# Performance work log

Hardware: AMD Instinct MI355X
Metric: run time of the kernel (lower is better)

The kernel has to match this reference:

```python
import jax, jax.numpy as jnp
import numpy as np

GAMMA = 0.96875


def setup_inputs() -> dict:
    key = jax.random.key(0)
    kx, kq, kk, kv = jax.random.split(key, 4)
    B, T, D = 4, 2048, 1024
    x = jax.random.normal(kx, (B, T, D), dtype=jnp.float32)
    Wq = jax.random.normal(kq, (D, D), dtype=jnp.float32) * (1.0 / np.sqrt(D))
    Wk = jax.random.normal(kk, (D, D), dtype=jnp.float32) * (1.0 / np.sqrt(D))
    Wv = jax.random.normal(kv, (D, D), dtype=jnp.float32) * (1.0 / np.sqrt(D))
    return {"x": x, "Wq": Wq, "Wk": Wk, "Wv": Wv}


def reference(x, Wq, Wk, Wv):
    # x: [B, T, D_in]; projections are bias-free Dense layers
    B, T, _ = x.shape
    D = Wq.shape[1]
    Q = jnp.einsum("bti,id->btd", x, Wq)  # [B,T,D]
    K = jnp.einsum("bti,id->btd", x, Wk)
    V = jnp.einsum("bti,id->btd", x, Wv)

    gamma = jnp.asarray(GAMMA, x.dtype)

    # Original: s[t] = gamma*s[t-1] + K[:,t,:]^T @ V[:,t,:]   (a [D,D] state,
    # batch is CONTRACTED by the matmul), then only reduce_sum over the last
    # state axis is used. The recurrence is linear, so it collapses exactly to
    # a [D]-vector recurrence with m_t[d] = sum_b K[b,t,d] * (sum_e V[b,t,e]).
    m = jnp.einsum("btd,bt->td", K, V.sum(axis=-1))  # [T,D]

    def step(s, mt):
        s_new = gamma * s + mt
        return s_new, s_new

    # loop runs t = 1..T-1 starting from s = 0; afterwards s[0] = s[1]
    _, states = jax.lax.scan(step, jnp.zeros((D,), x.dtype), m[1:])  # [T-1,D]
    S = jnp.concatenate([states[:1], states], axis=0)  # [T,D]

    # tf.reshape([T,D] -> [-1, T]) is a row-major element scramble, then transpose
    S = S.reshape(-1, T).T  # [T,D] (scrambled, faithful to the original)

    return S[None, :, :] * Q  # broadcast over batch -> [B,T,D]
```

## Files before the change

kernel.cpp:

```cpp
#include <hip/hip_runtime.h>
#include <hip/hip_bf16.h>
#include <cstddef>

#define T_DIM 2048
#define D_DIM 1024
#define GAMMA_F 0.96875f

typedef __attribute__((ext_vector_type(8))) short bf16x8;
typedef __attribute__((ext_vector_type(8))) ushort ushortx8;
typedef __attribute__((ext_vector_type(4))) float f32x4;

#define AS1 __attribute__((address_space(1)))
#define AS3 __attribute__((address_space(3)))

static __device__ inline ushort f2bs(float f) {
    __hip_bfloat16 h = __float2bfloat16(f);
    return *reinterpret_cast<ushort*>(&h);
}

template <int N>
static __device__ __forceinline__ void vm_wait() {
    if constexpr (N == 0)      asm volatile("s_waitcnt vmcnt(0)" ::: "memory");
    else if constexpr (N == 2) asm volatile("s_waitcnt vmcnt(2)" ::: "memory");
    else if constexpr (N == 3) asm volatile("s_waitcnt vmcnt(3)" ::: "memory");
    else if constexpr (N == 4) asm volatile("s_waitcnt vmcnt(4)" ::: "memory");
    else if constexpr (N == 6) asm volatile("s_waitcnt vmcnt(6)" ::: "memory");
    else if constexpr (N == 8) asm volatile("s_waitcnt vmcnt(8)" ::: "memory");
    else static_assert(N <= 8, "vmcnt");
}
static __device__ __forceinline__ void raw_barrier() {
    asm volatile("s_barrier" ::: "memory");
}

__global__ __launch_bounds__(256) void k_prep(const float* __restrict__ Wk,
                                              const float* __restrict__ Wq,
                                              const float* __restrict__ Wv,
                                              ushort* __restrict__ WTk,
                                              ushort* __restrict__ WTq,
                                              float* __restrict__ wv_sum) {
    const int tid = threadIdx.x;
    if (blockIdx.z == 2) {
        __shared__ float red[4];
        const int i = blockIdx.y * 32 + blockIdx.x;
        const float* row = Wv + (size_t)i * D_DIM;
        float p = 0.f;
        for (int c = tid; c < D_DIM; c += 256) p += row[c];
        for (int o = 32; o; o >>= 1) p += __shfl_down(p, o);
        if ((tid & 63) == 0) red[tid >> 6] = p;
        __syncthreads();
        if (tid == 0) wv_sum[i] = red[0] + red[1] + red[2] + red[3];
        return;
    }
    const float* W = (blockIdx.z == 0) ? Wk : Wq;
    ushort* WT     = (blockIdx.z == 0) ? WTk : WTq;
    __shared__ float tile[32][33];
    const int tx = tid & 31, ty = tid >> 5;
    const int kb = blockIdx.x * 32, nb = blockIdx.y * 32;
    #pragma unroll
    for (int r = 0; r < 4; ++r)
        tile[ty + 8 * r][tx] = W[(size_t)(kb + ty + 8 * r) * 1024 + nb + tx];
    __syncthreads();
    #pragma unroll
    for (int r = 0; r < 4; ++r)
        WT[(size_t)(nb + ty + 8 * r) * 1024 + kb + tx] =
            f2bs(tile[tx][ty + 8 * r]);
}

__global__ __launch_bounds__(256) void k_vsum_y(const float* __restrict__ x,
                                                const float* __restrict__ wv_sum,
                                                ushort* __restrict__ yb,
                                                ushort* __restrict__ xb) {
    __shared__ float xs[4][D_DIM];
    __shared__ float red[4][4];
    const int t = blockIdx.x;
    const int tid = threadIdx.x;
    const int lane = tid & 63, wv = tid >> 6;

    #pragma unroll
    for (int b = 0; b < 4; ++b) {
        const float4* xr = (const float4*)(x + ((size_t)b * T_DIM + t) * D_DIM);
        *(float4*)&xs[b][tid * 4] = xr[tid];
    }
    __syncthreads();

    #pragma unroll
    for (int b = 0; b < 4; ++b) {
        float p = 0.f;
        for (int c = tid; c < D_DIM; c += 256) p += xs[b][c] * wv_sum[c];
        for (int o = 32; o; o >>= 1) p += __shfl_down(p, o);
        if (lane == 0) red[wv][b] = p;
    }
    __syncthreads();

    float vs[4];
    #pragma unroll
    for (int b = 0; b < 4; ++b)
        vs[b] = red[0][b] + red[1][b] + red[2][b] + red[3][b];

    if (tid < 128) {
        const int i0 = tid * 8;
        ushortx8 yv;
        #pragma unroll
        for (int j = 0; j < 8; ++j) {
            float a = 0.f;
            #pragma unroll
            for (int b = 0; b < 4; ++b) a += xs[b][i0 + j] * vs[b];
            yv[j] = f2bs(a);
        }
        *(ushortx8*)(yb + (size_t)t * D_DIM + i0) = yv;
    }
    for (int g = tid; g < 512; g += 256) {
        const int b = g >> 7, i0 = (g & 127) * 8;
        ushortx8 xv;
        #pragma unroll
        for (int j = 0; j < 8; ++j) xv[j] = f2bs(xs[b][i0 + j]);
        *(ushortx8*)(xb + ((size_t)b * T_DIM + t) * D_DIM + i0) = xv;
    }
}

template <int MF, int NF, int EPI>
__global__ __launch_bounds__(512, 4) void k_gemm(const ushort* __restrict__ A,
                                                 const ushort* __restrict__ BT,
                                                 float* __restrict__ C,
                                                 const float* __restrict__ S2) {
    constexpr int BM = 4 * MF * 16;
    constexpr int BN = 2 * NF * 16;
    constexpr int LOADS = BM / 64 + BN / 64;
    __shared__ ushort As[2][BM][64];
    __shared__ ushort Bs[2][BN][64];
    const int tid = threadIdx.x;
    const int lane = tid & 63, wid = tid >> 6;
    const int wr = wid >> 1, wc = wid & 1;
    const int rowBase = blockIdx.x * BM;
    const int colBase = blockIdx.y * BN;

    f32x4 acc[MF][NF];
    #pragma unroll
    for (int i = 0; i < MF; ++i)
        #pragma unroll
        for (int j = 0; j < NF; ++j) acc[i][j] = f32x4{0.f, 0.f, 0.f, 0.f};

    auto stage = [&](int buf, int kb) {
        #pragma unroll
        for (int q = 0; q < BM / 64; ++q) {
            const int s = q * 8192 + tid * 16;
            const int r = s >> 7, grp = (s >> 4) & 7;
            const int gcol = kb + (((grp ^ (r & 7)) & 7) << 3);
            __builtin_amdgcn_global_load_lds(
                (const AS1 void*)(A + (size_t)(rowBase + r) * 1024 + gcol),
                (AS3 void*)((AS3 char*)&As[buf][0][0] + s), 16, 0, 0);
        }
        #pragma unroll
        for (int q = 0; q < BN / 64; ++q) {
            const int s = q * 8192 + tid * 16;
            const int r = s >> 7, grp = (s >> 4) & 7;
            const int gcol = kb + (((grp ^ (r & 7)) & 7) << 3);
            __builtin_amdgcn_global_load_lds(
                (const AS1 void*)(BT + (size_t)(colBase + r) * 1024 + gcol),
                (AS3 void*)((AS3 char*)&Bs[buf][0][0] + s), 16, 0, 0);
        }
    };

    stage(0, 0);

    #pragma unroll 2
    for (int kt = 0; kt < 16; ++kt) {
        const int cur = kt & 1;
        if (kt < 15) {
            stage(cur ^ 1, (kt + 1) * 64);
            vm_wait<LOADS>();
        } else {
            vm_wait<0>();
        }
        raw_barrier();

        bf16x8 af[2][MF], bfv[2][NF];
        #pragma unroll
        for (int ks = 0; ks < 2; ++ks) {
            const int kg = ks * 4 + (lane >> 4);
            #pragma unroll
            for (int mi = 0; mi < MF; ++mi) {
                const int r = wr * (MF * 16) + mi * 16 + (lane & 15);
                af[ks][mi] = *(const bf16x8*)((const char*)&As[cur][0][0] +
                                              r * 128 + (((kg ^ (r & 7)) & 7) << 4));
            }
            #pragma unroll
            for (int ni = 0; ni < NF; ++ni) {
                const int r = wc * (NF * 16) + ni * 16 + (lane & 15);
                bfv[ks][ni] = *(const bf16x8*)((const char*)&Bs[cur][0][0] +
                                               r * 128 + (((kg ^ (r & 7)) & 7) << 4));
            }
        }
        #pragma unroll
        for (int ks = 0; ks < 2; ++ks)
            #pragma unroll
            for (int mi = 0; mi < MF; ++mi)
                #pragma unroll
                for (int ni = 0; ni < NF; ++ni)
                    acc[mi][ni] = __builtin_amdgcn_mfma_f32_16x16x32_bf16(
                        af[ks][mi], bfv[ks][ni], acc[mi][ni], 0, 0, 0);

        asm volatile("s_waitcnt lgkmcnt(0)" ::: "memory");
        raw_barrier();
    }

    #pragma unroll
    for (int mi = 0; mi < MF; ++mi) {
        #pragma unroll
        for (int ni = 0; ni < NF; ++ni) {
            const int col = colBase + wc * (NF * 16) + ni * 16 + (lane & 15);
            #pragma unroll
            for (int q = 0; q < 4; ++q) {
                const int row = rowBase + wr * (MF * 16) + mi * 16 + (lane >> 4) * 4 + q;
                float v = acc[mi][ni][q];
                if (EPI)
                    v *= S2[(size_t)(row & (T_DIM - 1)) * D_DIM + col];
                C[(size_t)row * D_DIM + col] = v;
            }
        }
    }
}

#define SC_L 32
#define SC_NC 64

__global__ __launch_bounds__(256) void k_scan1(const float* __restrict__ m,
                                               float* __restrict__ tot) {
    const int col = blockIdx.x * 64 + (threadIdx.x & 63);
    const int ch  = blockIdx.y * 4 + (threadIdx.x >> 6);
    const int t0 = ch * SC_L;
    float r = 0.f;
    #pragma unroll 4
    for (int k = 0; k < SC_L; ++k) {
        const int t = t0 + k;
        const float a = (t == 0) ? 0.f : m[(size_t)t * D_DIM + col];
        r = GAMMA_F * r + a;
    }
    tot[(size_t)ch * D_DIM + col] = r;
}

__global__ __launch_bounds__(256) void k_scan2(const float* __restrict__ m,
                                               const float* __restrict__ tot,
                                               float* __restrict__ S2) {
    __shared__ float ls[128][65];
    const int tid = threadIdx.x;
    const int cl = tid & 63;
    const int ch = tid >> 6;
    const int col = blockIdx.x * 64 + cl;
    const int chg = blockIdx.y * 4 + ch;
    const int t0 = chg * SC_L;

    float gL = 1.f;
    #pragma unroll
    for (int i = 0; i < SC_L; ++i) gL *= GAMMA_F;

    float carry = 0.f, f = 1.f;
    for (int j = chg - 1; j >= 0; --j) {
        carry += f * tot[(size_t)j * D_DIM + col];
        f *= gL;
    }

    float r = carry, s1 = 0.f;
    #pragma unroll 4
    for (int k = 0; k < SC_L; ++k) {
        const int t = t0 + k;
        const float a = (t == 0) ? 0.f : m[(size_t)t * D_DIM + col];
        r = GAMMA_F * r + a;
        ls[ch * SC_L + k][cl] = r;
        if (t == 1) s1 = r;
    }
    if (blockIdx.y == 0 && ch == 0) ls[0][cl] = s1;
    __syncthreads();

    const int c0 = blockIdx.x * 64;
    const int tB = blockIdx.y * 128;
    for (int e = tid; e < 128 * 64; e += 256) {
        const int rr = e >> 6;
        const int j  = e & 63;
        const int hi = rr >> 6, cl2 = rr & 63;
        S2[(size_t)((hi << 10) + c0 + cl2) * D_DIM + (tB >> 1) + j] =
            ls[2 * j + hi][cl2];
    }
}

extern "C" void kernel_launch(void* const* d_in, const int* in_sizes, int n_in,
                              void* d_out, int out_size, void* d_ws, size_t ws_size,
                              hipStream_t stream) {
    const float* x  = (const float*)d_in[0];
    const float* Wq = (const float*)d_in[1];
    const float* Wk = (const float*)d_in[2];
    const float* Wv = (const float*)d_in[3];
    float* out = (float*)d_out;
    char* ws = (char*)d_ws;

    ushort* xb  = (ushort*)(ws);
    float*  m   = (float*)(ws + (16u << 20));
    ushort* yb  = (ushort*)(ws + (24u << 20));
    ushort* WTk = (ushort*)(ws + (28u << 20));
    ushort* WTq = (ushort*)(ws + (30u << 20));
    float*  S2  = (float*)(ws + (32u << 20));
    float*  wv_sum = m;
    float*  tot = (float*)yb;

    dim3 gP(32, 32, 3);
    k_prep<<<gP, 256, 0, stream>>>(Wk, Wq, Wv, WTk, WTq, wv_sum);

    k_vsum_y<<<T_DIM, 256, 0, stream>>>(x, wv_sum, (ushort*)yb, (ushort*)xb);

    dim3 gm(T_DIM / 128, D_DIM / 64);
    k_gemm<2, 2, 0><<<gm, 512, 0, stream>>>(yb, WTk, m, nullptr);

    dim3 gs(D_DIM / 64, SC_NC / 4);
    k_scan1<<<gs, 256, 0, stream>>>(m, tot);
    k_scan2<<<gs, 256, 0, stream>>>(m, tot, S2);

    dim3 gq((4 * T_DIM) / 128, D_DIM / 128);
    k_gemm<2, 4, 1><<<gq, 512, 0, stream>>>(xb, WTq, out, S2);
}
```

Measured before the change: 80.32 us.

## Add triple-buffered 256x128 GEMM kernel with interleaved loads for Q projection

Replaces the Q-projection GEMM with a new kernel that uses 256x128 output tiles, a three-stage LDS ring buffer filled by direct global-to-LDS loads, and phased MFMA blocks that interleave LDS reads, the next-stage prefetch and s_setprio raises. The aim is more data reuse per tile and better overlap of memory traffic with matrix math in the dominant GEMM. In exchange the larger LDS footprint and register use limit occupancy to two blocks per CU, and the grid is halved along rows. The original GEMM template loses its epilogue parameter and is kept only for the K projection.

```diff
diff --git a/kernel.cpp b/kernel.cpp
--- a/kernel.cpp
+++ b/kernel.cpp
@@ -20,16 +20,20 @@
 
 template <int N>
 static __device__ __forceinline__ void vm_wait() {
+    static_assert(N == 0 || N == 2 || N == 3 || N == 4 || N == 6 || N == 8,
+                  "vm_wait<N>: N not in emitted set");
     if constexpr (N == 0)      asm volatile("s_waitcnt vmcnt(0)" ::: "memory");
     else if constexpr (N == 2) asm volatile("s_waitcnt vmcnt(2)" ::: "memory");
     else if constexpr (N == 3) asm volatile("s_waitcnt vmcnt(3)" ::: "memory");
     else if constexpr (N == 4) asm volatile("s_waitcnt vmcnt(4)" ::: "memory");
     else if constexpr (N == 6) asm volatile("s_waitcnt vmcnt(6)" ::: "memory");
     else if constexpr (N == 8) asm volatile("s_waitcnt vmcnt(8)" ::: "memory");
-    else static_assert(N <= 8, "vmcnt");
 }
 static __device__ __forceinline__ void raw_barrier() {
     asm volatile("s_barrier" ::: "memory");
+}
+static __device__ __forceinline__ void lgkm0() {
+    asm volatile("s_waitcnt lgkmcnt(0)" ::: "memory");
 }
 
 __global__ __launch_bounds__(256) void k_prep(const float* __restrict__ Wk,
@@ -118,11 +122,10 @@
     }
 }
 
-template <int MF, int NF, int EPI>
+template <int MF, int NF>
 __global__ __launch_bounds__(512, 4) void k_gemm(const ushort* __restrict__ A,
                                                  const ushort* __restrict__ BT,
-                                                 float* __restrict__ C,
-                                                 const float* __restrict__ S2) {
+                                                 float* __restrict__ C) {
     constexpr int BM = 4 * MF * 16;
     constexpr int BN = 2 * NF * 16;
     constexpr int LOADS = BM / 64 + BN / 64;
@@ -200,7 +203,7 @@
                     acc[mi][ni] = __builtin_amdgcn_mfma_f32_16x16x32_bf16(
                         af[ks][mi], bfv[ks][ni], acc[mi][ni], 0, 0, 0);
 
-        asm volatile("s_waitcnt lgkmcnt(0)" ::: "memory");
+        lgkm0();
         raw_barrier();
     }
 
@@ -212,6 +215,145 @@
             #pragma unroll
             for (int q = 0; q < 4; ++q) {
                 const int row = rowBase + wr * (MF * 16) + mi * 16 + (lane >> 4) * 4 + q;
+                C[(size_t)row * D_DIM + col] = acc[mi][ni][q];
+            }
+        }
+    }
+}
+
+template <int EPI>
+__global__ __launch_bounds__(512, 2) void k_gemm8(const ushort* __restrict__ A,
+                                                  const ushort* __restrict__ BT,
+                                                  float* __restrict__ C,
+                                                  const float* __restrict__ S2) {
+    constexpr int ABYTES = 256 * 64 * 2;
+    constexpr int BBYTES = 128 * 64 * 2;
+    constexpr int TBYTES = ABYTES + BBYTES;
+    __shared__ char lds[3 * TBYTES];
+    const int tid = threadIdx.x;
+    const int lane = tid & 63, wid = tid >> 6;
+    const int wr = wid >> 1, wc = wid & 1;
+    const int rowBase = blockIdx.x * 256;
+    const int colBase = blockIdx.y * 128;
+
+    f32x4 acc[4][4];
+    #pragma unroll
+    for (int i = 0; i < 4; ++i)
+        #pragma unroll
+        for (int j = 0; j < 4; ++j) acc[i][j] = f32x4{0.f, 0.f, 0.f, 0.f};
+
+    auto stage_part = [&](int buf, int kb, int p) {
+        #pragma unroll
+        for (int qq = 0; qq < 2; ++qq) {
+            const int s = (p * 2 + qq) * 8192 + tid * 16;
+            const int r = s >> 7, grp = (s >> 4) & 7;
+            const int gcol = kb + (((grp ^ (r & 7)) & 7) << 3);
+            __builtin_amdgcn_global_load_lds(
+                (const AS1 void*)(A + (size_t)(rowBase + r) * 1024 + gcol),
+                (AS3 void*)((AS3 char*)lds + buf * TBYTES + s), 16, 0, 0);
+        }
+        {
+            const int s = p * 8192 + tid * 16;
+            const int r = s >> 7, grp = (s >> 4) & 7;
+            const int gcol = kb + (((grp ^ (r & 7)) & 7) << 3);
+            __builtin_amdgcn_global_load_lds(
+                (const AS1 void*)(BT + (size_t)(colBase + r) * 1024 + gcol),
+                (AS3 void*)((AS3 char*)lds + buf * TBYTES + ABYTES + s), 16, 0, 0);
+        }
+    };
+
+    auto rdA = [&](int buf, int mi, int kg) -> bf16x8 {
+        const int r = wr * 64 + mi * 16 + (lane & 15);
+        return *(const bf16x8*)((const char*)lds + buf * TBYTES +
+                                r * 128 + (((kg ^ (r & 7)) & 7) << 4));
+    };
+    auto rdB = [&](int buf, int ni, int kg) -> bf16x8 {
+        const int r = wc * 64 + ni * 16 + (lane & 15);
+        return *(const bf16x8*)((const char*)lds + buf * TBYTES + ABYTES +
+                                r * 128 + (((kg ^ (r & 7)) & 7) << 4));
+    };
+
+    stage_part(0, 0, 0);  stage_part(0, 0, 1);
+    stage_part(1, 64, 0); stage_part(1, 64, 1);
+    vm_wait<6>();
+    raw_barrier();
+
+    const int kg0 = (lane >> 4);
+    const int kg1 = 4 + (lane >> 4);
+    int cur = 0;
+
+    #pragma unroll 1
+    for (int kt = 0; kt < 16; ++kt) {
+        int b2 = cur + 2; if (b2 >= 3) b2 -= 3;
+        const int kb2 = (kt + 2) * 64;
+
+        bf16x8 af[2][4], bfv[2][4];
+
+        af[0][0] = rdA(cur, 0, kg0); af[0][1] = rdA(cur, 1, kg0);
+        af[1][0] = rdA(cur, 0, kg1); af[1][1] = rdA(cur, 1, kg1);
+        bfv[0][0] = rdB(cur, 0, kg0); bfv[0][1] = rdB(cur, 1, kg0);
+        bfv[1][0] = rdB(cur, 0, kg1); bfv[1][1] = rdB(cur, 1, kg1);
+        if (kt < 14) stage_part(b2, kb2, 0);
+        raw_barrier();
+        lgkm0();
+        __builtin_amdgcn_s_setprio(1);
+        #pragma unroll
+        for (int ks = 0; ks < 2; ++ks)
+            #pragma unroll
+            for (int mi = 0; mi < 2; ++mi)
+                #pragma unroll
+                for (int ni = 0; ni < 2; ++ni)
+                    acc[mi][ni] = __builtin_amdgcn_mfma_f32_16x16x32_bf16(
+                        af[ks][mi], bfv[ks][ni], acc[mi][ni], 0, 0, 0);
+        __builtin_amdgcn_s_setprio(0);
+        raw_barrier();
+
+        bfv[0][2] = rdB(cur, 2, kg0); bfv[0][3] = rdB(cur, 3, kg0);
+        bfv[1][2] = rdB(cur, 2, kg1); bfv[1][3] = rdB(cur, 3, kg1);
+        if (kt < 14) stage_part(b2, kb2, 1);
+        raw_barrier();
+        lgkm0();
+        __builtin_amdgcn_s_setprio(1);
+        #pragma unroll
+        for (int ks = 0; ks < 2; ++ks)
+            #pragma unroll
+            for (int mi = 0; mi < 2; ++mi)
+                #pragma unroll
+                for (int ni = 2; ni < 4; ++ni)
+                    acc[mi][ni] = __builtin_amdgcn_mfma_f32_16x16x32_bf16(
+                        af[ks][mi], bfv[ks][ni], acc[mi][ni], 0, 0, 0);
+        __builtin_amdgcn_s_setprio(0);
+        raw_barrier();
+
+        af[0][2] = rdA(cur, 2, kg0); af[0][3] = rdA(cur, 3, kg0);
+        af[1][2] = rdA(cur, 2, kg1); af[1][3] = rdA(cur, 3, kg1);
+        raw_barrier();
+        lgkm0();
+        __builtin_amdgcn_s_setprio(1);
+        #pragma unroll
+        for (int ks = 0; ks < 2; ++ks)
+            #pragma unroll
+            for (int mi = 2; mi < 4; ++mi)
+                #pragma unroll
+                for (int ni = 0; ni < 4; ++ni)
+                    acc[mi][ni] = __builtin_amdgcn_mfma_f32_16x16x32_bf16(
+                        af[ks][mi], bfv[ks][ni], acc[mi][ni], 0, 0, 0);
+        __builtin_amdgcn_s_setprio(0);
+        if (kt < 14)       vm_wait<6>();
+        else if (kt == 14) vm_wait<0>();
+        raw_barrier();
+
+        cur += 1; if (cur == 3) cur = 0;
+    }
+
+    #pragma unroll
+    for (int mi = 0; mi < 4; ++mi) {
+        #pragma unroll
+        for (int ni = 0; ni < 4; ++ni) {
+            const int col = colBase + wc * 64 + ni * 16 + (lane & 15);
+            #pragma unroll
+            for (int q = 0; q < 4; ++q) {
+                const int row = rowBase + wr * 64 + mi * 16 + (lane >> 4) * 4 + q;
                 float v = acc[mi][ni][q];
                 if (EPI)
                     v *= S2[(size_t)(row & (T_DIM - 1)) * D_DIM + col];
@@ -308,12 +450,12 @@
     k_vsum_y<<<T_DIM, 256, 0, stream>>>(x, wv_sum, (ushort*)yb, (ushort*)xb);
 
     dim3 gm(T_DIM / 128, D_DIM / 64);
-    k_gemm<2, 2, 0><<<gm, 512, 0, stream>>>(yb, WTk, m, nullptr);
+    k_gemm<2, 2><<<gm, 512, 0, stream>>>(yb, WTk, m);
 
     dim3 gs(D_DIM / 64, SC_NC / 4);
     k_scan1<<<gs, 256, 0, stream>>>(m, tot);
     k_scan2<<<gs, 256, 0, stream>>>(m, tot, S2);
 
-    dim3 gq((4 * T_DIM) / 128, D_DIM / 128);
-    k_gemm<2, 4, 1><<<gq, 512, 0, stream>>>(xb, WTq, out, S2);
-}
+    dim3 gq((4 * T_DIM) / 256, D_DIM / 128);
+    k_gemm8<1><<<gq, 512, 0, stream>>>(xb, WTq, out, S2);
+}
```

New measurement: 81.61 us. No clear change (+1.6%).

## Merge two-pass chunked scan into one kernel with redundant prefix recompute

Applied to the files above, without the earlier changes.

Replaces the two-kernel chunked scan (per-chunk totals, then carry propagation) with a single kernel where each thread recomputes its carry by scanning m serially from t=1 up to its chunk start. This removes one kernel launch and the intermediate totals buffer. In exchange, work grows quadratically with chunk index: late chunks serially read up to about 2048 rows per column, which lengthens the critical path, and the redundant reads go through cache.

```diff
diff --git a/kernel.cpp b/kernel.cpp
--- a/kernel.cpp
+++ b/kernel.cpp
@@ -20,16 +20,20 @@
 
 template <int N>
 static __device__ __forceinline__ void vm_wait() {
+    static_assert(N == 0 || N == 2 || N == 3 || N == 4 || N == 6 || N == 8,
+                  "vm_wait<N>: N not in emitted set");
     if constexpr (N == 0)      asm volatile("s_waitcnt vmcnt(0)" ::: "memory");
     else if constexpr (N == 2) asm volatile("s_waitcnt vmcnt(2)" ::: "memory");
     else if constexpr (N == 3) asm volatile("s_waitcnt vmcnt(3)" ::: "memory");
     else if constexpr (N == 4) asm volatile("s_waitcnt vmcnt(4)" ::: "memory");
     else if constexpr (N == 6) asm volatile("s_waitcnt vmcnt(6)" ::: "memory");
     else if constexpr (N == 8) asm volatile("s_waitcnt vmcnt(8)" ::: "memory");
-    else static_assert(N <= 8, "vmcnt");
 }
 static __device__ __forceinline__ void raw_barrier() {
     asm volatile("s_barrier" ::: "memory");
+}
+static __device__ __forceinline__ void lgkm0() {
+    asm volatile("s_waitcnt lgkmcnt(0)" ::: "memory");
 }
 
 __global__ __launch_bounds__(256) void k_prep(const float* __restrict__ Wk,
@@ -200,7 +204,7 @@
                     acc[mi][ni] = __builtin_amdgcn_mfma_f32_16x16x32_bf16(
                         af[ks][mi], bfv[ks][ni], acc[mi][ni], 0, 0, 0);
 
-        asm volatile("s_waitcnt lgkmcnt(0)" ::: "memory");
+        lgkm0();
         raw_barrier();
     }
 
@@ -222,26 +226,9 @@
 }
 
 #define SC_L 32
-#define SC_NC 64
-
-__global__ __launch_bounds__(256) void k_scan1(const float* __restrict__ m,
-                                               float* __restrict__ tot) {
-    const int col = blockIdx.x * 64 + (threadIdx.x & 63);
-    const int ch  = blockIdx.y * 4 + (threadIdx.x >> 6);
-    const int t0 = ch * SC_L;
-    float r = 0.f;
-    #pragma unroll 4
-    for (int k = 0; k < SC_L; ++k) {
-        const int t = t0 + k;
-        const float a = (t == 0) ? 0.f : m[(size_t)t * D_DIM + col];
-        r = GAMMA_F * r + a;
-    }
-    tot[(size_t)ch * D_DIM + col] = r;
-}
-
-__global__ __launch_bounds__(256) void k_scan2(const float* __restrict__ m,
-                                               const float* __restrict__ tot,
-                                               float* __restrict__ S2) {
+
+__global__ __launch_bounds__(256) void k_scan(const float* __restrict__ m,
+                                              float* __restrict__ S2) {
     __shared__ float ls[128][65];
     const int tid = threadIdx.x;
     const int cl = tid & 63;
@@ -250,17 +237,25 @@
     const int chg = blockIdx.y * 4 + ch;
     const int t0 = chg * SC_L;
 
-    float gL = 1.f;
-    #pragma unroll
-    for (int i = 0; i < SC_L; ++i) gL *= GAMMA_F;
-
-    float carry = 0.f, f = 1.f;
-    for (int j = chg - 1; j >= 0; --j) {
-        carry += f * tot[(size_t)j * D_DIM + col];
-        f *= gL;
-    }
-
-    float r = carry, s1 = 0.f;
+    float r = 0.f;
+    {
+        const float* mc = m + col;
+        int tau = 1;
+        for (; tau + 3 < t0; tau += 4) {
+            float a0 = mc[(size_t)(tau + 0) * D_DIM];
+            float a1 = mc[(size_t)(tau + 1) * D_DIM];
+            float a2 = mc[(size_t)(tau + 2) * D_DIM];
+            float a3 = mc[(size_t)(tau + 3) * D_DIM];
+            r = GAMMA_F * r + a0;
+            r = GAMMA_F * r + a1;
+            r = GAMMA_F * r + a2;
+            r = GAMMA_F * r + a3;
+        }
+        for (; tau < t0; ++tau)
+            r = GAMMA_F * r + mc[(size_t)tau * D_DIM];
+    }
+
+    float s1 = 0.f;
     #pragma unroll 4
     for (int k = 0; k < SC_L; ++k) {
         const int t = t0 + k;
@@ -300,7 +295,6 @@
     ushort* WTq = (ushort*)(ws + (30u << 20));
     float*  S2  = (float*)(ws + (32u << 20));
     float*  wv_sum = m;
-    float*  tot = (float*)yb;
 
     dim3 gP(32, 32, 3);
     k_prep<<<gP, 256, 0, stream>>>(Wk, Wq, Wv, WTk, WTq, wv_sum);
@@ -310,9 +304,8 @@
     dim3 gm(T_DIM / 128, D_DIM / 64);
     k_gemm<2, 2, 0><<<gm, 512, 0, stream>>>(yb, WTk, m, nullptr);
 
-    dim3 gs(D_DIM / 64, SC_NC / 4);
-    k_scan1<<<gs, 256, 0, stream>>>(m, tot);
-    k_scan2<<<gs, 256, 0, stream>>>(m, tot, S2);
+    dim3 gs(D_DIM / 64, T_DIM / 128);
+    k_scan<<<gs, 256, 0, stream>>>(m, S2);
 
     dim3 gq((4 * T_DIM) / 128, D_DIM / 128);
     k_gemm<2, 4, 1><<<gq, 512, 0, stream>>>(xb, WTq, out, S2);
```

Result: slower. 237.8 us (+196.1%).

## Fuse chunk-level scan totals into the K-projection GEMM epilogue

Applied to the files above, without the earlier changes.

Removes the separate k_scan1 kernel. Each wave of the first GEMM now computes its 32-row chunk's decayed sum from the accumulator registers, using gamma-power weights and cross-lane shuffles, and writes it to a dedicated tot buffer. This saves a kernel launch and a full re-read of m, at the cost of extra epilogue math. It also makes the result depend on the chunk size matching the GEMM wave tile, and it special-cases the t=0 row.

```diff
diff --git a/kernel.cpp b/kernel.cpp
--- a/kernel.cpp
+++ b/kernel.cpp
@@ -18,18 +18,28 @@
     return *reinterpret_cast<ushort*>(&h);
 }
 
+constexpr float gpw(int n) {
+    float r = 1.f;
+    for (int i = 0; i < n; ++i) r *= GAMMA_F;
+    return r;
+}
+
 template <int N>
 static __device__ __forceinline__ void vm_wait() {
+    static_assert(N == 0 || N == 2 || N == 3 || N == 4 || N == 6 || N == 8,
+                  "vm_wait<N>: N not in emitted set");
     if constexpr (N == 0)      asm volatile("s_waitcnt vmcnt(0)" ::: "memory");
     else if constexpr (N == 2) asm volatile("s_waitcnt vmcnt(2)" ::: "memory");
     else if constexpr (N == 3) asm volatile("s_waitcnt vmcnt(3)" ::: "memory");
     else if constexpr (N == 4) asm volatile("s_waitcnt vmcnt(4)" ::: "memory");
     else if constexpr (N == 6) asm volatile("s_waitcnt vmcnt(6)" ::: "memory");
     else if constexpr (N == 8) asm volatile("s_waitcnt vmcnt(8)" ::: "memory");
-    else static_assert(N <= 8, "vmcnt");
 }
 static __device__ __forceinline__ void raw_barrier() {
     asm volatile("s_barrier" ::: "memory");
+}
+static __device__ __forceinline__ void lgkm0() {
+    asm volatile("s_waitcnt lgkmcnt(0)" ::: "memory");
 }
 
 __global__ __launch_bounds__(256) void k_prep(const float* __restrict__ Wk,
@@ -118,11 +128,13 @@
     }
 }
 
-template <int MF, int NF, int EPI>
+template <int MF, int NF, int MODE>
 __global__ __launch_bounds__(512, 4) void k_gemm(const ushort* __restrict__ A,
                                                  const ushort* __restrict__ BT,
                                                  float* __restrict__ C,
-                                                 const float* __restrict__ S2) {
+                                                 const float* __restrict__ S2,
+                                                 float* __restrict__ tot) {
+    static_assert(MODE != 0 || MF == 2, "fused scan1 requires 32-row wave tiles");
     constexpr int BM = 4 * MF * 16;
     constexpr int BN = 2 * NF * 16;
     constexpr int LOADS = BM / 64 + BN / 64;
@@ -200,7 +212,7 @@
                     acc[mi][ni] = __builtin_amdgcn_mfma_f32_16x16x32_bf16(
                         af[ks][mi], bfv[ks][ni], acc[mi][ni], 0, 0, 0);
 
-        asm volatile("s_waitcnt lgkmcnt(0)" ::: "memory");
+        lgkm0();
         raw_barrier();
     }
 
@@ -213,31 +225,40 @@
             for (int q = 0; q < 4; ++q) {
                 const int row = rowBase + wr * (MF * 16) + mi * 16 + (lane >> 4) * 4 + q;
                 float v = acc[mi][ni][q];
-                if (EPI)
+                if (MODE == 1)
                     v *= S2[(size_t)(row & (T_DIM - 1)) * D_DIM + col];
                 C[(size_t)row * D_DIM + col] = v;
             }
         }
     }
+
+    if (MODE == 0) {
+        const int h = lane >> 4;
+        const int t3 = 3 - h;
+        const float A0 = ((t3 & 1) ? gpw(4) : 1.f) * ((t3 & 2) ? gpw(8) : 1.f);
+        const int chunk = blockIdx.x * 4 + wr;
+        #pragma unroll
+        for (int ni = 0; ni < NF; ++ni) {
+            float part = 0.f;
+            #pragma unroll
+            for (int mi = 0; mi < MF; ++mi)
+                #pragma unroll
+                for (int q = 0; q < 4; ++q)
+                    part += (A0 * gpw(16 * (MF - 1 - mi) + (3 - q))) * acc[mi][ni][q];
+            if (chunk == 0 && h == 0)
+                part -= (A0 * gpw(16 * (MF - 1) + 3)) * acc[0][ni][0];
+            part += __shfl_xor(part, 16);
+            part += __shfl_xor(part, 32);
+            if (h == 0) {
+                const int col = colBase + wc * (NF * 16) + ni * 16 + (lane & 15);
+                tot[(size_t)chunk * D_DIM + col] = part;
+            }
+        }
+    }
 }
 
 #define SC_L 32
 #define SC_NC 64
-
-__global__ __launch_bounds__(256) void k_scan1(const float* __restrict__ m,
-                                               float* __restrict__ tot) {
-    const int col = blockIdx.x * 64 + (threadIdx.x & 63);
-    const int ch  = blockIdx.y * 4 + (threadIdx.x >> 6);
-    const int t0 = ch * SC_L;
-    float r = 0.f;
-    #pragma unroll 4
-    for (int k = 0; k < SC_L; ++k) {
-        const int t = t0 + k;
-        const float a = (t == 0) ? 0.f : m[(size_t)t * D_DIM + col];
-        r = GAMMA_F * r + a;
-    }
-    tot[(size_t)ch * D_DIM + col] = r;
-}
 
 __global__ __launch_bounds__(256) void k_scan2(const float* __restrict__ m,
                                                const float* __restrict__ tot,
@@ -250,9 +271,7 @@
     const int chg = blockIdx.y * 4 + ch;
     const int t0 = chg * SC_L;
 
-    float gL = 1.f;
-    #pragma unroll
-    for (int i = 0; i < SC_L; ++i) gL *= GAMMA_F;
+    constexpr float gL = gpw(SC_L);
 
     float carry = 0.f, f = 1.f;
     for (int j = chg - 1; j >= 0; --j) {
@@ -299,8 +318,8 @@
     ushort* WTk = (ushort*)(ws + (28u << 20));
     ushort* WTq = (ushort*)(ws + (30u << 20));
     float*  S2  = (float*)(ws + (32u << 20));
+    float*  tot = (float*)(ws + (40u << 20));
     float*  wv_sum = m;
-    float*  tot = (float*)yb;
 
     dim3 gP(32, 32, 3);
     k_prep<<<gP, 256, 0, stream>>>(Wk, Wq, Wv, WTk, WTq, wv_sum);
@@ -308,12 +327,11 @@
     k_vsum_y<<<T_DIM, 256, 0, stream>>>(x, wv_sum, (ushort*)yb, (ushort*)xb);
 
     dim3 gm(T_DIM / 128, D_DIM / 64);
-    k_gemm<2, 2, 0><<<gm, 512, 0, stream>>>(yb, WTk, m, nullptr);
+    k_gemm<2, 2, 0><<<gm, 512, 0, stream>>>(yb, WTk, m, nullptr, tot);
 
     dim3 gs(D_DIM / 64, SC_NC / 4);
-    k_scan1<<<gs, 256, 0, stream>>>(m, tot);
     k_scan2<<<gs, 256, 0, stream>>>(m, tot, S2);
 
     dim3 gq((4 * T_DIM) / 128, D_DIM / 128);
-    k_gemm<2, 4, 1><<<gq, 512, 0, stream>>>(xb, WTq, out, S2);
-}
+    k_gemm<2, 4, 1><<<gq, 512, 0, stream>>>(xb, WTq, out, S2, nullptr);
+}
```

New measurement: 78.02 us. 2.9% less time.
